# Kernel optimization log

Measured on AMD Instinct MI355X. Metric: run time of the kernel, lower is better.

The kernel has to match this reference:

```python
import jax, jax.numpy as jnp
import numpy as np

SEQ, BS, DIM = 2048, 2, 256
G, NQ = 2, 8           # n_keys groups, n_queries total
SUB = NQ // G          # queries per group
EPS = 1e-5


def _ln(x, gamma, beta):
    m = jnp.mean(x, axis=-1, keepdims=True)
    v = jnp.mean(jnp.square(x - m), axis=-1, keepdims=True)
    return (x - m) * jax.lax.rsqrt(v + EPS) * gamma + beta


def setup_inputs() -> dict:
    key = jax.random.key(0)
    ks = jax.random.split(key, 16)
    s = 0.02
    return {
        "x":   jax.random.normal(ks[0], (SEQ, BS, DIM), jnp.float32),
        # block layernorms
        "g0": jnp.ones((DIM,), jnp.float32), "b0": jnp.zeros((DIM,), jnp.float32),
        "g1": jnp.ones((DIM,), jnp.float32), "b1": jnp.zeros((DIM,), jnp.float32),
        # attention q/k layernorm (norm_kvs=True)
        "gn": jnp.ones((DIM,), jnp.float32), "bn": jnp.zeros((DIM,), jnp.float32),
        # attention projections (torch Linear: weight [out,in])
        "wk": jax.random.normal(ks[1], (DIM * G, DIM), jnp.float32) * s,
        "bk": jnp.zeros((DIM * G,), jnp.float32),
        "wv": jax.random.normal(ks[2], (DIM * G, DIM), jnp.float32) * s,
        "bv": jnp.zeros((DIM * G,), jnp.float32),
        "wq": jax.random.normal(ks[3], (DIM * NQ, DIM), jnp.float32) * s,
        "bq": jnp.zeros((DIM * NQ,), jnp.float32),
        "wo": jax.random.normal(ks[4], (DIM, DIM * NQ), jnp.float32) * s,
        "bo": jnp.zeros((DIM,), jnp.float32),
        # FFN: BayesLora(dim,2dim) -> relu -> BayesLora(2dim,dim), eval == plain linear
        "w1": jax.random.normal(ks[5], (2 * DIM, DIM), jnp.float32) * s,
        "bf1": jnp.zeros((2 * DIM,), jnp.float32),
        "w2": jax.random.normal(ks[6], (DIM, 2 * DIM), jnp.float32) * s,
        "bf2": jnp.zeros((DIM,), jnp.float32),
    }


def reference(x, g0, b0, g1, b1, gn, bn, wk, bk, wv, bv, wq, bq, wo, bo, w1, bf1, w2, bf2):
    seq, bs, dim = x.shape
    # --- attention (pre-norm) ---
    h = _ln(x, g0, b0)                                        # s b d
    K = (h @ wk.T + bk).reshape(seq, bs, G, dim)              # s b g i
    V = (h @ wv.T + bv).reshape(seq, bs, G, dim)              # s b g i
    Q = (h @ wq.T + bq).reshape(seq, bs, G, SUB, dim)         # s b g u i
    K = _ln(K, gn, bn)
    Q = _ln(Q, gn, bn)
    scores = jnp.einsum('sbgui,tbgi->bgust', Q, K) / jnp.sqrt(jnp.float32(dim))
    neg = jnp.finfo(scores.dtype).min
    causal = jnp.tril(jnp.ones((seq, seq), bool))             # s1 >= s2 allowed
    scores = jnp.where(causal, scores, neg)
    probs = jax.nn.softmax(scores, axis=-1)                   # b g u s t
    out = jnp.einsum('bgust,tbgi->sbgui', probs, V)
    out = out.reshape(seq, bs, G * SUB * dim)                 # s b (g u i)
    x = x + (out @ wo.T + bo)
    # --- FFN (pre-norm) ---
    h2 = _ln(x, g1, b1)
    f = jax.nn.relu(h2 @ w1.T + bf1) @ w2.T + bf2
    return x + f
```

## Files before the change

### kernel.cpp

```cpp
#include <hip/hip_runtime.h>
#include <hip/hip_bf16.h>

#define SEQ  2048
#define BSZ  2
#define DIM  256
#define NG   2
#define NQH  8
#define SUBQ 4
#define ROWS (SEQ*BSZ)
#define NQKV 3072
#define QROW 6144

typedef unsigned int uint32;
typedef unsigned short ushort;
typedef __attribute__((ext_vector_type(8))) short short8;
typedef __attribute__((ext_vector_type(4))) float f32x4;

__device__ __forceinline__ float bflo(uint32 u){
  union { uint32 i; float f; } c; c.i = u << 16; return c.f;
}
__device__ __forceinline__ float bfhi(uint32 u){
  union { uint32 i; float f; } c; c.i = u & 0xffff0000u; return c.f;
}
__device__ __forceinline__ uint32 pack2(float a, float b){
  __hip_bfloat16 ha = __float2bfloat16(a);
  __hip_bfloat16 hb = __float2bfloat16(b);
  unsigned short ua, ub;
  __builtin_memcpy(&ua, &ha, 2);
  __builtin_memcpy(&ub, &hb, 2);
  return (uint32)ua | ((uint32)ub << 16);
}
__device__ __forceinline__ ushort bf16bits(float v){
  __hip_bfloat16 h = __float2bfloat16(v);
  ushort u; __builtin_memcpy(&u, &h, 2); return u;
}

__device__ __forceinline__ void dma16(const void* g, void* l) {
  __builtin_amdgcn_global_load_lds(
      (const __attribute__((address_space(1))) uint32*)g,
      (__attribute__((address_space(3))) uint32*)l, 16, 0, 0);
}

__device__ __forceinline__ size_t op2_addr(size_t o2) {
  return (o2 >> 11) * QROW + (o2 & 1023) + ((o2 >> 10) & 1) * 3072;
}

__global__ __launch_bounds__(256) void misc0(
    const float* __restrict__ wk, const float* __restrict__ wv,
    const float* __restrict__ wq, const float* __restrict__ wo,
    const float* __restrict__ w1, const float* __restrict__ w2,
    const float* __restrict__ bk, const float* __restrict__ bv,
    const float* __restrict__ bq,
    __hip_bfloat16* __restrict__ out, float* __restrict__ bc,
    const float* __restrict__ x, const float* __restrict__ g0,
    const float* __restrict__ b0, __hip_bfloat16* __restrict__ Hf)
{
  if (blockIdx.x < 771) {
    int u = blockIdx.x * 256 + threadIdx.x;
    if (u < 196608) {
      int lane = u & 63, col = lane & 15, quad = lane >> 4;
      const float* srcrow;
      if (u < 98304) {
        int n16 = u >> 9, kc = (u >> 6) & 7;
        int n = n16 * 16 + col;
        const float* m = (n < 512) ? (wk + (size_t)n * 256)
                       : (n < 1024) ? (wv + (size_t)(n - 512) * 256)
                                    : (wq + (size_t)(n - 1024) * 256);
        srcrow = m + kc * 32 + quad * 8;
      } else if (u < 163840) {
        int local = u - 98304;
        int n16 = local >> 12, kc = (local >> 6) & 63;
        srcrow = wo + (size_t)(n16 * 16 + col) * 2048 + kc * 32 + quad * 8;
      } else if (u < 180224) {
        int local = u - 163840;
        int n16 = local >> 9, kc = (local >> 6) & 7;
        srcrow = w1 + (size_t)(n16 * 16 + col) * 256 + kc * 32 + quad * 8;
      } else {
        int local = u - 180224;
        int n16 = local >> 10, kc = (local >> 6) & 15;
        srcrow = w2 + (size_t)(n16 * 16 + col) * 512 + kc * 32 + quad * 8;
      }
      float4 a = *(const float4*)srcrow;
      float4 b = *(const float4*)(srcrow + 4);
      uint4 st;
      st.x = pack2(a.x, a.y); st.y = pack2(a.z, a.w);
      st.z = pack2(b.x, b.y); st.w = pack2(b.z, b.w);
      *(uint4*)((ushort*)out + (size_t)u * 8) = st;
    } else {
      int bu = u - 196608;
      const float* src; int loc;
      if      (bu < 128) { src = bk; loc = bu; }
      else if (bu < 256) { src = bv; loc = bu - 128; }
      else               { src = bq; loc = bu - 256; }
      *(float4*)(bc + 4 * (size_t)bu) = *(const float4*)(src + 4 * (size_t)loc);
    }
  } else {
    int wave = threadIdx.x >> 6, lane = threadIdx.x & 63;
    int row = (blockIdx.x - 771) * 4 + wave;
    size_t base = (size_t)row * DIM + lane * 4;
    float4 v = *(const float4*)(x + base);
    float s  = v.x + v.y + v.z + v.w;
    float s2 = v.x*v.x + v.y*v.y + v.z*v.z + v.w*v.w;
    #pragma unroll
    for (int o = 1; o < 64; o <<= 1) {
      s  += __shfl_xor(s, o);
      s2 += __shfl_xor(s2, o);
    }
    float m = s * (1.0f / DIM);
    float rb = rsqrtf(s2 * (1.0f / DIM) - m * m + 1e-5f);
    float4 gm = *(const float4*)(g0 + lane * 4);
    float4 bt = *(const float4*)(b0 + lane * 4);
    uint2 st;
    st.x = pack2((v.x - m) * rb * gm.x + bt.x, (v.y - m) * rb * gm.y + bt.y);
    st.y = pack2((v.z - m) * rb * gm.z + bt.z, (v.w - m) * rb * gm.w + bt.w);
    int kc = lane >> 3, quad = (lane >> 1) & 3, jj = 4 * (lane & 1);
    int cid = (row >> 4) * 8 + kc;
    *(uint2*)((ushort*)Hf + (size_t)cid * 512 + (quad * 16 + (row & 15)) * 8 + jj) = st;
  }
}

__global__ __launch_bounds__(256) void ln_swz(
    __hip_bfloat16* __restrict__ QKV,
    const float* __restrict__ gamma, const float* __restrict__ beta,
    __hip_bfloat16* __restrict__ Kf, __hip_bfloat16* __restrict__ Vf)
{
  int j = blockIdx.x;
  if (j < 10240) {
    int wave = threadIdx.x >> 6, lane = threadIdx.x & 63;
    int idx = j * 4 + wave;
    size_t base;
    if (idx < 8192) base = (size_t)(idx >> 1) * NQKV + (idx & 1) * DIM;
    else {
      int qi = idx - 8192;
      base = (size_t)(qi >> 3) * NQKV + 2 * NG * DIM + (qi & 7) * DIM;
    }
    __hip_bfloat16* p = QKV + base + lane * 4;
    uint2 u = *(const uint2*)p;
    float v0 = bflo(u.x), v1 = bfhi(u.x), v2 = bflo(u.y), v3 = bfhi(u.y);
    float s  = v0 + v1 + v2 + v3;
    float s2 = v0*v0 + v1*v1 + v2*v2 + v3*v3;
    #pragma unroll
    for (int o = 1; o < 64; o <<= 1) {
      s  += __shfl_xor(s, o);
      s2 += __shfl_xor(s2, o);
    }
    float m = s * (1.0f / DIM);
    float rb = rsqrtf(s2 * (1.0f / DIM) - m * m + 1e-5f);
    float4 gm = *(const float4*)(gamma + lane * 4);
    float4 bt = *(const float4*)(beta + lane * 4);
    uint2 st;
    st.x = pack2((v0 - m) * rb * gm.x + bt.x, (v1 - m) * rb * gm.y + bt.y);
    st.y = pack2((v2 - m) * rb * gm.z + bt.z, (v3 - m) * rb * gm.w + bt.w);
    if (idx < 8192) {
      int r = idx >> 1, gg = idx & 1;
      int t = r >> 1, b = r & 1;
      int bg = b * NG + gg;
      int kt = t >> 5, tr = t & 31, tc = tr >> 4, col = tr & 15;
      int ks = lane >> 3, quad = (lane >> 1) & 3, jj = 4 * (lane & 1);
      int cid = (bg * 64 + kt) * 16 + tc * 8 + ks;
      *(uint2*)((ushort*)Kf + (size_t)cid * 512 + (quad * 16 + col) * 8 + jj) = st;
    } else {
      *(uint2*)p = st;
    }
  } else {
    __shared__ ushort T[64][72];
    int vb = j - 10240;
    int t0 = (vb & 31) * 64, d0 = ((vb >> 5) & 3) * 64, bg = vb >> 7;
    int b = bg >> 1, g = bg & 1;
    int tid = threadIdx.x;
    int tr = tid >> 2, c4 = (tid & 3) * 16;
    const ushort* src = (const ushort*)QKV + ((size_t)(t0 + tr) * BSZ + b) * NQKV
                      + NG * DIM + g * DIM + d0 + c4;
    uint4 a0 = *(const uint4*)src;
    uint4 a1 = *(const uint4*)(src + 8);
    *(uint4*)&T[tr][c4]     = a0;
    *(uint4*)&T[tr][c4 + 8] = a1;
    __syncthreads();
    #pragma unroll
    for (int k2 = 0; k2 < 2; ++k2) {
      int u = tid * 2 + k2;
      int tt = u >> 8, di = (u >> 6) & 3, qd = (u >> 4) & 3, cl = u & 15;
      ushort tmp[8];
      #pragma unroll
      for (int e = 0; e < 8; ++e) tmp[e] = T[tt * 32 + qd * 8 + e][di * 16 + cl];
      int kt = (t0 >> 5) + tt;
      int dc = (d0 >> 4) + di;
      *(uint4*)((ushort*)Vf + (((size_t)(bg * 64 + kt) * 16 + dc) << 9) + (qd * 16 + cl) * 8)
          = *(uint4*)tmp;
    }
  }
}

template<int GN, int RELU, int OUTMODE, int AFRAG>
__global__ __launch_bounds__(256) void gemm_mfma(
    const __hip_bfloat16* __restrict__ A,
    const __hip_bfloat16* __restrict__ W,
    const float* __restrict__ bias,
    const float* __restrict__ resid,
    void* __restrict__ outp,
    int M, int N, int K)
{
  constexpr int WCH = GN / 16;
  constexpr int MC  = (GN == 128) ? 4 : 2;
  __shared__ __align__(16) ushort AS[2][4096];
  __shared__ __align__(16) ushort WS[2][WCH * 512];

  const int tid = threadIdx.x;
  const int wave = tid >> 6, lane = tid & 63;
  const int col = lane & 15, quad = lane >> 4;
  const int wm = (GN == 128) ? (wave >> 1) : wave;
  const int wn = (GN == 128) ? (wave & 1) : 0;
  const int bn0 = blockIdx.x * GN;
  const int bm0 = blockIdx.y * 128;
  const bool SPLIT = (OUTMODE == 2 || OUTMODE == 4);
  const int Keff  = SPLIT ? (K / gridDim.z) : K;
  const int kbase = SPLIT ? blockIdx.z * Keff : 0;
  const int kiters = Keff >> 5;

  f32x4 acc[MC][4];
  #pragma unroll
  for (int mc = 0; mc < MC; ++mc)
    #pragma unroll
    for (int nc = 0; nc < 4; ++nc)
      acc[mc][nc] = (f32x4){0.f, 0.f, 0.f, 0.f};

  auto stage = [&](int it, int bufi) {
    int k0 = kbase + it * 32;
    #pragma unroll
    for (int c = 0; c < 2; ++c) {
      int ch = wave * 2 + c;
      if (AFRAG)
        dma16((const ushort*)A + ((((size_t)(bm0 >> 4) + ch) * (K >> 5) + (k0 >> 5)) << 9) + lane * 8,
              &AS[bufi][ch * 512]);
      else
        dma16((const ushort*)A + (size_t)(bm0 + ch * 16 + col) * K + k0 + quad * 8,
              &AS[bufi][ch * 512]);
    }
    #pragma unroll
    for (int c = 0; c < WCH / 4; ++c) {
      int ch = wave * (WCH / 4) + c;
      dma16((const ushort*)W + (((size_t)((bn0 >> 4) + ch) * (K >> 5) + (k0 >> 5)) << 9) + lane * 8,
            &WS[bufi][ch * 512]);
    }
  };

  stage(0, 0);
  for (int it = 0; it < kiters; ++it) {
    int cur = it & 1;
    __syncthreads();
    if (it + 1 < kiters) stage(it + 1, 1 - cur);
    short8 af[MC], bf_[4];
    #pragma unroll
    for (int mc = 0; mc < MC; ++mc)
      af[mc] = *(const short8*)&AS[cur][(wm * MC + mc) * 512 + lane * 8];
    #pragma unroll
    for (int nc = 0; nc < 4; ++nc)
      bf_[nc] = *(const short8*)&WS[cur][(wn * 4 + nc) * 512 + lane * 8];
    #pragma unroll
    for (int mc = 0; mc < MC; ++mc)
      #pragma unroll
      for (int nc = 0; nc < 4; ++nc)
        acc[mc][nc] = __builtin_amdgcn_mfma_f32_16x16x32_bf16(af[mc], bf_[nc], acc[mc][nc], 0, 0, 0);
  }

  #pragma unroll
  for (int nc = 0; nc < 4; ++nc) {
    int n = bn0 + wn * 64 + nc * 16 + col;
    float bv = 0.f;
    if (OUTMODE == 0 || OUTMODE == 1 || OUTMODE == 3) bv = bias[n];
    #pragma unroll
    for (int mc = 0; mc < MC; ++mc) {
      #pragma unroll
      for (int reg = 0; reg < 4; ++reg) {
        int m = bm0 + wm * (MC * 16) + mc * 16 + quad * 4 + reg;
        float v = acc[mc][nc][reg] + bv;
        if ((OUTMODE == 0 || OUTMODE == 1 || OUTMODE == 3) && resid)
          v += resid[(size_t)m * N + n];
        if (RELU) v = fmaxf(v, 0.f);
        if (OUTMODE == 0)
          ((__hip_bfloat16*)outp)[(size_t)m * N + n] = __float2bfloat16(v);
        else if (OUTMODE == 1)
          ((float*)outp)[(size_t)m * N + n] = v;
        else if (OUTMODE == 2)
          ((float*)outp)[(size_t)blockIdx.z * M * N + (size_t)m * N + n] = v;
        else if (OUTMODE == 3) {
          int cid = (m >> 4) * (N >> 5) + (n >> 5);
          int kl = n & 31;
          ((ushort*)outp)[(size_t)cid * 512 + ((kl >> 3) * 16 + (m & 15)) * 8 + (kl & 7)] = bf16bits(v);
        } else {
          ((ushort*)outp)[(size_t)blockIdx.z * M * N + (size_t)m * N + n] = bf16bits(v);
        }
      }
    }
  }
}

__global__ __launch_bounds__(256) void combine2(
    const ushort* __restrict__ P, const float* __restrict__ bias,
    const float* __restrict__ resid, float* __restrict__ out, int MN)
{
  int i4 = (blockIdx.x * 256 + threadIdx.x) * 4;
  uint2 a = *(const uint2*)(P + i4);
  uint2 b = *(const uint2*)(P + MN + i4);
  float4 r = *(const float4*)(resid + i4);
  float4 bb = *(const float4*)(bias + (i4 & (DIM - 1)));
  float4 o;
  o.x = bflo(a.x) + bflo(b.x) + r.x + bb.x;
  o.y = bfhi(a.x) + bfhi(b.x) + r.y + bb.y;
  o.z = bflo(a.y) + bflo(b.y) + r.z + bb.z;
  o.w = bfhi(a.y) + bfhi(b.y) + r.w + bb.w;
  *(float4*)(out + i4) = o;
}

__global__ __launch_bounds__(256) void combine_ln4(
    const ushort* __restrict__ P, const float* __restrict__ bias,
    const float* __restrict__ resid, float* __restrict__ X2,
    const float* __restrict__ gamma, const float* __restrict__ beta,
    __hip_bfloat16* __restrict__ H2f)
{
  const int MN = ROWS * DIM;
  int wave = threadIdx.x >> 6, lane = threadIdx.x & 63;
  int row = blockIdx.x * 4 + wave;
  size_t i = (size_t)row * DIM + lane * 4;
  uint2 a = *(const uint2*)(P + i);
  uint2 b = *(const uint2*)(P + MN + i);
  uint2 c = *(const uint2*)(P + 2 * (size_t)MN + i);
  uint2 d = *(const uint2*)(P + 3 * (size_t)MN + i);
  float4 r = *(const float4*)(resid + i);
  float4 bb = *(const float4*)(bias + lane * 4);
  float4 v;
  v.x = bflo(a.x) + bflo(b.x) + bflo(c.x) + bflo(d.x) + r.x + bb.x;
  v.y = bfhi(a.x) + bfhi(b.x) + bfhi(c.x) + bfhi(d.x) + r.y + bb.y;
  v.z = bflo(a.y) + bflo(b.y) + bflo(c.y) + bflo(d.y) + r.z + bb.z;
  v.w = bfhi(a.y) + bfhi(b.y) + bfhi(c.y) + bfhi(d.y) + r.w + bb.w;
  *(float4*)(X2 + i) = v;
  float s  = v.x + v.y + v.z + v.w;
  float s2 = v.x*v.x + v.y*v.y + v.z*v.z + v.w*v.w;
  #pragma unroll
  for (int o = 1; o < 64; o <<= 1) {
    s  += __shfl_xor(s, o);
    s2 += __shfl_xor(s2, o);
  }
  float m = s * (1.0f / DIM);
  float rb = rsqrtf(s2 * (1.0f / DIM) - m * m + 1e-5f);
  float4 gm = *(const float4*)(gamma + lane * 4);
  float4 bt = *(const float4*)(beta + lane * 4);
  uint2 st;
  st.x = pack2((v.x - m) * rb * gm.x + bt.x, (v.y - m) * rb * gm.y + bt.y);
  st.y = pack2((v.z - m) * rb * gm.z + bt.z, (v.w - m) * rb * gm.w + bt.w);
  int kc = lane >> 3, quad = (lane >> 1) & 3, jj = 4 * (lane & 1);
  int cid = (row >> 4) * 8 + kc;
  *(uint2*)((ushort*)H2f + (size_t)cid * 512 + (quad * 16 + (row & 15)) * 8 + jj) = st;
}

__constant__ int C_NIT[32] = {22,22,22,21,21,20,20,20,20,20,20,19,19,18,18,18,18,17,17,16,16,16,16,16,16,14,14,12,12,12, 8, 4};
__constant__ int C_QB [32] = {10,10,15,15,15, 4, 9, 9,14,14,14,13,13,13, 8, 8,12,12,12, 3, 7, 7,11,11,11, 6, 6, 2, 5, 5, 1, 0};
__constant__ int C_Z  [32] = { 0, 1, 0, 1, 2, 0, 0, 1, 0, 1, 2, 0, 1, 2, 0, 1, 0, 1, 2, 0, 0, 1, 0, 1, 2, 0, 1, 0, 0, 1, 0, 0};
__constant__ int C_K0 [32] = { 0,22, 0,22,43, 0, 0,20, 0,20,40, 0,19,38, 0,18, 0,18,35, 0, 0,16, 0,16,32, 0,14, 0, 0,12, 0, 0};
__constant__ int C_SP [32] = { 1, 1, 1, 1, 1, 0, 1, 1, 1, 1, 1, 1, 1, 1, 1, 1, 1, 1, 1, 0, 1, 1, 1, 1, 1, 1, 1, 0, 1, 1, 0, 0};

__global__ __launch_bounds__(256, 2) void attn_mfma(
    const __hip_bfloat16* QKV,
    const __hip_bfloat16* __restrict__ Kf,
    const __hip_bfloat16* __restrict__ Vf,
    __hip_bfloat16* __restrict__ Obf,
    __hip_bfloat16* __restrict__ Op1f,
    ushort* Op2q,
    float* __restrict__ Lp)
{
  __shared__ __align__(16) ushort KS[2][8192];
  __shared__ __align__(16) ushort VS[2][8192];
  __shared__ __align__(16) ushort Pw[4][1280];

  const int tid  = threadIdx.x;
  const int wave = tid >> 6, lane = tid & 63;
  const int col  = lane & 15, quad = lane >> 4;

  const int bid = blockIdx.x;
  const int x8 = bid & 7, j = bid >> 3;
  const int a = j >> 1, odd = j & 1;
  int rank;
  if (a < 16) rank = odd ? (31 - a) : a;
  else        rank = odd ? (a - 16) : (31 - (a - 16));
  const int head = odd * 8 + x8;
  const int qb  = C_QB[rank];
  const int z   = C_Z[rank];
  const int nit = C_NIT[rank];
  const int k0  = C_K0[rank];
  const int split = C_SP[rank];

  const int b = head >> 3, hq = head & 7, g = hq >> 2;
  const int bg = b * NG + g;
  const int qw0 = qb * 128 + wave * 32;

  short8 qf[2][8];
  #pragma unroll
  for (int mc = 0; mc < 2; ++mc) {
    int s = qw0 + mc * 16 + col;
    const ushort* qp = (const ushort*)QKV + (size_t)s * QROW + b * NQKV
                     + 2 * NG * DIM + hq * DIM + quad * 8;
    #pragma unroll
    for (int ks = 0; ks < 8; ++ks)
      qf[mc][ks] = *(const short8*)(qp + ks * 32);
  }

  short8 onesf;
  #pragma unroll
  for (int i = 0; i < 8; ++i) onesf[i] = (short)0x3F80;

  f32x4 o[2][16];
  #pragma unroll
  for (int mc = 0; mc < 2; ++mc)
    #pragma unroll
    for (int dc = 0; dc < 16; ++dc)
      o[mc][dc] = (f32x4){0.f, 0.f, 0.f, 0.f};
  float l_s[2][4] = {{0.f}};

  auto stage = [&](int i, int bufi) {
    int kt = k0 + i;
    const ushort* kb = (const ushort*)Kf + (((size_t)bg * 64 + kt) << 13);
    const ushort* vb = (const ushort*)Vf + (((size_t)bg * 64 + kt) << 13);
    #pragma unroll
    for (int cc = 0; cc < 4; ++cc) {
      int nk = wave * 4 + cc;
      dma16(kb + (nk << 9) + lane * 8, &KS[bufi][nk * 512]);
      dma16(vb + (nk << 9) + lane * 8, &VS[bufi][nk * 512]);
    }
  };

  stage(0, 0);
  for (int i = 0; i < nit; ++i) {
    int cur = i & 1;
    __syncthreads();
    if (i + 1 < nit) stage(i + 1, 1 - cur);
    int kt = k0 + i;
    if (kt * 32 > qw0 + 31) continue;

    f32x4 sf[2][2];
    #pragma unroll
    for (int mc = 0; mc < 2; ++mc)
      #pragma unroll
      for (int tc = 0; tc < 2; ++tc)
        sf[mc][tc] = (f32x4){0.f, 0.f, 0.f, 0.f};
    #pragma unroll
    for (int ks = 0; ks < 8; ++ks) {
      short8 kb0 = *(const short8*)&KS[cur][ks * 512 + lane * 8];
      short8 kb1 = *(const short8*)&KS[cur][(8 + ks) * 512 + lane * 8];
      sf[0][0] = __builtin_amdgcn_mfma_f32_16x16x32_bf16(qf[0][ks], kb0, sf[0][0], 0, 0, 0);
      sf[0][1] = __builtin_amdgcn_mfma_f32_16x16x32_bf16(qf[0][ks], kb1, sf[0][1], 0, 0, 0);
      sf[1][0] = __builtin_amdgcn_mfma_f32_16x16x32_bf16(qf[1][ks], kb0, sf[1][0], 0, 0, 0);
      sf[1][1] = __builtin_amdgcn_mfma_f32_16x16x32_bf16(qf[1][ks], kb1, sf[1][1], 0, 0, 0);
    }

    const bool dm = (kt * 32 + 31) > qw0;
    #pragma unroll
    for (int mc = 0; mc < 2; ++mc)
      #pragma unroll
      for (int tc = 0; tc < 2; ++tc)
        #pragma unroll
        for (int reg = 0; reg < 4; ++reg) {
          float p = __expf(sf[mc][tc][reg] * 0.0625f);
          if (dm) {
            int tg = kt * 32 + tc * 16 + col;
            int sg = qw0 + mc * 16 + quad * 4 + reg;
            if (tg > sg) p = 0.f;
          }
          Pw[wave][(mc * 16 + quad * 4 + reg) * 40 + tc * 16 + col] = bf16bits(p);
        }

    short8 pa0 = *(const short8*)&Pw[wave][col * 40 + quad * 8];
    short8 pa1 = *(const short8*)&Pw[wave][(16 + col) * 40 + quad * 8];

    f32x4 zz = (f32x4){0.f, 0.f, 0.f, 0.f};
    f32x4 ps0 = __builtin_amdgcn_mfma_f32_16x16x32_bf16(pa0, onesf, zz, 0, 0, 0);
    f32x4 ps1 = __builtin_amdgcn_mfma_f32_16x16x32_bf16(pa1, onesf, zz, 0, 0, 0);
    #pragma unroll
    for (int r = 0; r < 4; ++r) { l_s[0][r] += ps0[r]; l_s[1][r] += ps1[r]; }

    #pragma unroll
    for (int dc = 0; dc < 16; ++dc) {
      short8 vb = *(const short8*)&VS[cur][dc * 512 + lane * 8];
      o[0][dc] = __builtin_amdgcn_mfma_f32_16x16x32_bf16(pa0, vb, o[0][dc], 0, 0, 0);
      o[1][dc] = __builtin_amdgcn_mfma_f32_16x16x32_bf16(pa1, vb, o[1][dc], 0, 0, 0);
    }
  }

  const int colh = col >> 3, coll = col & 7;
  #pragma unroll
  for (int mc = 0; mc < 2; ++mc)
    #pragma unroll
    for (int reg = 0; reg < 4; ++reg) {
      int s = qw0 + mc * 16 + quad * 4 + reg;
      int m = s * BSZ + b;
      int m16 = m >> 4, ml = m & 15;
      if (!split) {
        float inv = 1.0f / l_s[mc][reg];
        #pragma unroll
        for (int dc = 0; dc < 16; ++dc) {
          int cid = m16 * 64 + hq * 8 + (dc >> 1);
          int qt = (dc & 1) * 2 + colh;
          Obf[(size_t)cid * 512 + (qt * 16 + ml) * 8 + coll] =
              __float2bfloat16(o[mc][dc][reg] * inv);
        }
      } else {
        #pragma unroll
        for (int dc = 0; dc < 16; ++dc) {
          int qt = (dc & 1) * 2 + colh;
          int el = (qt * 16 + ml) * 8 + coll;
          float v = o[mc][dc][reg];
          if (z == 0) {
            Obf[((size_t)(m16 * 64 + hq * 8 + (dc >> 1))) * 512 + el] = __float2bfloat16(v);
          } else if (z == 1) {
            Op1f[((size_t)((m16 - 80) * 64 + hq * 8 + (dc >> 1))) * 512 + el] = __float2bfloat16(v);
          } else {
            size_t o2 = ((size_t)((m16 - 176) * 64 + hq * 8 + (dc >> 1))) * 512 + el;
            Op2q[op2_addr(o2)] = bf16bits(v);
          }
        }
        if (col == 0) Lp[((size_t)z * 2048 + s) * 16 + head] = l_s[mc][reg];
      }
    }
}

__global__ __launch_bounds__(256) void attn_norm(
    __hip_bfloat16* __restrict__ Obf, const __hip_bfloat16* __restrict__ Op1f,
    const ushort* __restrict__ Op2q, const float* __restrict__ Lp)
{
  int i8 = blockIdx.x * 256 + threadIdx.x;
  int cidr = i8 >> 6;
  int lane = i8 & 63;
  int m16r = cidr >> 6, kc = cidr & 63;
  int m16 = m16r + 80;
  int m = m16 * 16 + (lane & 15);
  int k = kc * 32 + (lane >> 4) * 8;
  int s = m >> 1, b = m & 1, hq = k >> 8;
  int head = b * 8 + hq;
  float l = Lp[(size_t)s * 16 + head] + Lp[(size_t)(2048 + s) * 16 + head];
  ushort* a = (ushort*)Obf + (((size_t)m16 * 64 + kc) << 9) + lane * 8;
  const ushort* c = (const ushort*)Op1f + (((size_t)m16r * 64 + kc) << 9) + lane * 8;
  uint4 ua = *(const uint4*)a;
  uint4 uc = *(const uint4*)c;
  float v0 = bflo(ua.x) + bflo(uc.x), v1 = bfhi(ua.x) + bfhi(uc.x);
  float v2 = bflo(ua.y) + bflo(uc.y), v3 = bfhi(ua.y) + bfhi(uc.y);
  float v4 = bflo(ua.z) + bflo(uc.z), v5 = bfhi(ua.z) + bfhi(uc.z);
  float v6 = bflo(ua.w) + bflo(uc.w), v7 = bfhi(ua.w) + bfhi(uc.w);
  if (s >= 1408) {
    l += Lp[(size_t)(4096 + s) * 16 + head];
    size_t o2 = (((size_t)(m16 - 176) * 64 + kc) << 9) + lane * 8;
    uint4 ue = *(const uint4*)(Op2q + op2_addr(o2));
    v0 += bflo(ue.x); v1 += bfhi(ue.x);
    v2 += bflo(ue.y); v3 += bfhi(ue.y);
    v4 += bflo(ue.z); v5 += bfhi(ue.z);
    v6 += bflo(ue.w); v7 += bfhi(ue.w);
  }
  float inv = 1.0f / l;
  uint4 st;
  st.x = pack2(v0 * inv, v1 * inv);
  st.y = pack2(v2 * inv, v3 * inv);
  st.z = pack2(v4 * inv, v5 * inv);
  st.w = pack2(v6 * inv, v7 * inv);
  *(uint4*)a = st;
}

extern "C" void kernel_launch(void* const* d_in, const int* in_sizes, int n_in,
                              void* d_out, int out_size, void* d_ws, size_t ws_size,
                              hipStream_t stream)
{
  const float* x   = (const float*)d_in[0];
  const float* g0  = (const float*)d_in[1];
  const float* b0  = (const float*)d_in[2];
  const float* g1  = (const float*)d_in[3];
  const float* b1  = (const float*)d_in[4];
  const float* gn  = (const float*)d_in[5];
  const float* bn  = (const float*)d_in[6];
  const float* wk  = (const float*)d_in[7];
  const float* bk  = (const float*)d_in[8];
  const float* wv  = (const float*)d_in[9];
  const float* bv  = (const float*)d_in[10];
  const float* wq  = (const float*)d_in[11];
  const float* bq  = (const float*)d_in[12];
  const float* wo  = (const float*)d_in[13];
  const float* bo  = (const float*)d_in[14];
  const float* w1  = (const float*)d_in[15];
  const float* bf1 = (const float*)d_in[16];
  const float* w2  = (const float*)d_in[17];
  const float* bf2 = (const float*)d_in[18];

  char* ws = (char*)d_ws;
  const size_t MB = 1024 * 1024;
  __hip_bfloat16* QKV = (__hip_bfloat16*)(ws);
  __hip_bfloat16* Pwo = (__hip_bfloat16*)(ws);
  __hip_bfloat16* Pw2 = (__hip_bfloat16*)(ws + 8  * MB);
  float*          X2  = (float*)         (ws + 16 * MB);
  __hip_bfloat16* H2f = (__hip_bfloat16*)(ws + 20 * MB);
  __hip_bfloat16* F1f = (__hip_bfloat16*)(ws + 22 * MB);
  __hip_bfloat16* Hf  = (__hip_bfloat16*)(ws + 24 * MB);
  __hip_bfloat16* Kf  = (__hip_bfloat16*)(ws + 24 * MB);
  __hip_bfloat16* Vf  = (__hip_bfloat16*)(ws + 28 * MB);
  __hip_bfloat16* Obf = (__hip_bfloat16*)(ws + 32 * MB);
  __hip_bfloat16* Op1f= (__hip_bfloat16*)(ws + 48 * MB);
  float*          BC  = (float*)         (ws + 59 * MB);
  float*          Lp  = (float*)         (ws + 59 * MB + 64 * 1024);
  __hip_bfloat16* WB  = (__hip_bfloat16*)(ws + 61 * MB);

  __hip_bfloat16* woB = WB + 786432;
  __hip_bfloat16* w1B = WB + 1310720;
  __hip_bfloat16* w2B = WB + 1441792;

  misc0<<<1795, 256, 0, stream>>>(wk, wv, wq, wo, w1, w2, bk, bv, bq, WB, BC, x, g0, b0, Hf);
  gemm_mfma<128,0,0,1><<<dim3(NQKV/128, ROWS/128), 256, 0, stream>>>(Hf, WB, BC, nullptr, QKV, ROWS, NQKV, DIM);
  ln_swz<<<12288, 256, 0, stream>>>(QKV, gn, bn, Kf, Vf);
  attn_mfma<<<512, 256, 0, stream>>>(QKV, Kf, Vf, Obf, Op1f, (ushort*)QKV, Lp);
  attn_norm<<<2816, 256, 0, stream>>>(Obf, Op1f, (const ushort*)QKV, Lp);
  gemm_mfma<64,0,4,1><<<dim3(DIM/64, ROWS/128, 4), 256, 0, stream>>>(Obf, woB, nullptr, nullptr, Pwo, ROWS, DIM, NQH*DIM);
  combine_ln4<<<ROWS / 4, 256, 0, stream>>>((const ushort*)Pwo, bo, x, X2, g1, b1, H2f);
  gemm_mfma<64,1,3,1><<<dim3((2*DIM)/64, ROWS/128), 256, 0, stream>>>(H2f, w1B, bf1, nullptr, F1f, ROWS, 2*DIM, DIM);
  gemm_mfma<64,0,4,1><<<dim3(DIM/64, ROWS/128, 2), 256, 0, stream>>>(F1f, w2B, nullptr, nullptr, Pw2, ROWS, DIM, 2*DIM);
  combine2<<<ROWS*DIM/1024, 256, 0, stream>>>((const ushort*)Pw2, bf2, X2, (float*)d_out, ROWS*DIM);
}
```

Measured before the change: 241.9 us.

## Fuse Q layernorm into attention kernel and raise MFMA wave priority

Removes the Q-layernorm pass from ln_swz (grid shrinks from 12288 to 4096 blocks) and instead normalizes Q fragments in registers at the start of attn_mfma, using cross-lane shuffles for mean and variance. This drops a read-modify-write of the 16 MB Q region of the QKV buffer. It also wraps the QK and PV MFMA loops in s_setprio(1)/s_setprio(0) so waves issuing matrix ops get scheduler priority. The cost is that each attention block recomputes Q norms, and the extra gamma/beta loads add some register pressure.

Result: slower. 253.8 us (+4.9%).

```diff
diff --git a/kernel.cpp b/kernel.cpp
--- a/kernel.cpp
+++ b/kernel.cpp
@@ -21,6 +21,9 @@
 }
 __device__ __forceinline__ float bfhi(uint32 u){
   union { uint32 i; float f; } c; c.i = u & 0xffff0000u; return c.f;
+}
+__device__ __forceinline__ float bfu(ushort u){
+  union { uint32 i; float f; } c; c.i = (uint32)u << 16; return c.f;
 }
 __device__ __forceinline__ uint32 pack2(float a, float b){
   __hip_bfloat16 ha = __float2bfloat16(a);
@@ -125,15 +128,10 @@
     __hip_bfloat16* __restrict__ Kf, __hip_bfloat16* __restrict__ Vf)
 {
   int j = blockIdx.x;
-  if (j < 10240) {
+  if (j < 2048) {
     int wave = threadIdx.x >> 6, lane = threadIdx.x & 63;
     int idx = j * 4 + wave;
-    size_t base;
-    if (idx < 8192) base = (size_t)(idx >> 1) * NQKV + (idx & 1) * DIM;
-    else {
-      int qi = idx - 8192;
-      base = (size_t)(qi >> 3) * NQKV + 2 * NG * DIM + (qi & 7) * DIM;
-    }
+    size_t base = (size_t)(idx >> 1) * NQKV + (idx & 1) * DIM;
     __hip_bfloat16* p = QKV + base + lane * 4;
     uint2 u = *(const uint2*)p;
     float v0 = bflo(u.x), v1 = bfhi(u.x), v2 = bflo(u.y), v3 = bfhi(u.y);
@@ -151,20 +149,16 @@
     uint2 st;
     st.x = pack2((v0 - m) * rb * gm.x + bt.x, (v1 - m) * rb * gm.y + bt.y);
     st.y = pack2((v2 - m) * rb * gm.z + bt.z, (v3 - m) * rb * gm.w + bt.w);
-    if (idx < 8192) {
-      int r = idx >> 1, gg = idx & 1;
-      int t = r >> 1, b = r & 1;
-      int bg = b * NG + gg;
-      int kt = t >> 5, tr = t & 31, tc = tr >> 4, col = tr & 15;
-      int ks = lane >> 3, quad = (lane >> 1) & 3, jj = 4 * (lane & 1);
-      int cid = (bg * 64 + kt) * 16 + tc * 8 + ks;
-      *(uint2*)((ushort*)Kf + (size_t)cid * 512 + (quad * 16 + col) * 8 + jj) = st;
-    } else {
-      *(uint2*)p = st;
-    }
+    int r = idx >> 1, gg = idx & 1;
+    int t = r >> 1, b = r & 1;
+    int bg = b * NG + gg;
+    int kt = t >> 5, tr = t & 31, tc = tr >> 4, col = tr & 15;
+    int ks = lane >> 3, quad = (lane >> 1) & 3, jj = 4 * (lane & 1);
+    int cid = (bg * 64 + kt) * 16 + tc * 8 + ks;
+    *(uint2*)((ushort*)Kf + (size_t)cid * 512 + (quad * 16 + col) * 8 + jj) = st;
   } else {
     __shared__ ushort T[64][72];
-    int vb = j - 10240;
+    int vb = j - 2048;
     int t0 = (vb & 31) * 64, d0 = ((vb >> 5) & 3) * 64, bg = vb >> 7;
     int b = bg >> 1, g = bg & 1;
     int tid = threadIdx.x;
@@ -363,6 +357,7 @@
     const __hip_bfloat16* QKV,
     const __hip_bfloat16* __restrict__ Kf,
     const __hip_bfloat16* __restrict__ Vf,
+    const float* __restrict__ gn, const float* __restrict__ bn,
     __hip_bfloat16* __restrict__ Obf,
     __hip_bfloat16* __restrict__ Op1f,
     ushort* Op2q,
@@ -402,6 +397,32 @@
     #pragma unroll
     for (int ks = 0; ks < 8; ++ks)
       qf[mc][ks] = *(const short8*)(qp + ks * 32);
+    float sm = 0.f, s2 = 0.f;
+    #pragma unroll
+    for (int ks = 0; ks < 8; ++ks)
+      #pragma unroll
+      for (int jj = 0; jj < 8; ++jj) {
+        float f = bfu((ushort)qf[mc][ks][jj]);
+        sm += f; s2 += f * f;
+      }
+    sm += __shfl_xor(sm, 16); s2 += __shfl_xor(s2, 16);
+    sm += __shfl_xor(sm, 32); s2 += __shfl_xor(s2, 32);
+    float mm = sm * (1.0f / DIM);
+    float rb = rsqrtf(s2 * (1.0f / DIM) - mm * mm + 1e-5f);
+    #pragma unroll
+    for (int ks = 0; ks < 8; ++ks) {
+      float4 ga = *(const float4*)(gn + ks * 32 + quad * 8);
+      float4 gb = *(const float4*)(gn + ks * 32 + quad * 8 + 4);
+      float4 ba = *(const float4*)(bn + ks * 32 + quad * 8);
+      float4 bb = *(const float4*)(bn + ks * 32 + quad * 8 + 4);
+      float gg[8] = {ga.x, ga.y, ga.z, ga.w, gb.x, gb.y, gb.z, gb.w};
+      float bt[8] = {ba.x, ba.y, ba.z, ba.w, bb.x, bb.y, bb.z, bb.w};
+      short8 q = qf[mc][ks];
+      #pragma unroll
+      for (int jj = 0; jj < 8; ++jj)
+        q[jj] = (short)bf16bits((bfu((ushort)q[jj]) - mm) * rb * gg[jj] + bt[jj]);
+      qf[mc][ks] = q;
+    }
   }
 
   short8 onesf;
@@ -442,6 +463,7 @@
       #pragma unroll
       for (int tc = 0; tc < 2; ++tc)
         sf[mc][tc] = (f32x4){0.f, 0.f, 0.f, 0.f};
+    __builtin_amdgcn_s_setprio(1);
     #pragma unroll
     for (int ks = 0; ks < 8; ++ks) {
       short8 kb0 = *(const short8*)&KS[cur][ks * 512 + lane * 8];
@@ -451,6 +473,7 @@
       sf[1][0] = __builtin_amdgcn_mfma_f32_16x16x32_bf16(qf[1][ks], kb0, sf[1][0], 0, 0, 0);
       sf[1][1] = __builtin_amdgcn_mfma_f32_16x16x32_bf16(qf[1][ks], kb1, sf[1][1], 0, 0, 0);
     }
+    __builtin_amdgcn_s_setprio(0);
 
     const bool dm = (kt * 32 + 31) > qw0;
     #pragma unroll
@@ -471,6 +494,7 @@
     short8 pa0 = *(const short8*)&Pw[wave][col * 40 + quad * 8];
     short8 pa1 = *(const short8*)&Pw[wave][(16 + col) * 40 + quad * 8];
 
+    __builtin_amdgcn_s_setprio(1);
     f32x4 zz = (f32x4){0.f, 0.f, 0.f, 0.f};
     f32x4 ps0 = __builtin_amdgcn_mfma_f32_16x16x32_bf16(pa0, onesf, zz, 0, 0, 0);
     f32x4 ps1 = __builtin_amdgcn_mfma_f32_16x16x32_bf16(pa1, onesf, zz, 0, 0, 0);
@@ -483,6 +507,7 @@
       o[0][dc] = __builtin_amdgcn_mfma_f32_16x16x32_bf16(pa0, vb, o[0][dc], 0, 0, 0);
       o[1][dc] = __builtin_amdgcn_mfma_f32_16x16x32_bf16(pa1, vb, o[1][dc], 0, 0, 0);
     }
+    __builtin_amdgcn_s_setprio(0);
   }
 
   const int colh = col >> 3, coll = col & 7;
@@ -609,8 +634,8 @@
 
   misc0<<<1795, 256, 0, stream>>>(wk, wv, wq, wo, w1, w2, bk, bv, bq, WB, BC, x, g0, b0, Hf);
   gemm_mfma<128,0,0,1><<<dim3(NQKV/128, ROWS/128), 256, 0, stream>>>(Hf, WB, BC, nullptr, QKV, ROWS, NQKV, DIM);
-  ln_swz<<<12288, 256, 0, stream>>>(QKV, gn, bn, Kf, Vf);
-  attn_mfma<<<512, 256, 0, stream>>>(QKV, Kf, Vf, Obf, Op1f, (ushort*)QKV, Lp);
+  ln_swz<<<4096, 256, 0, stream>>>(QKV, gn, bn, Kf, Vf);
+  attn_mfma<<<512, 256, 0, stream>>>(QKV, Kf, Vf, gn, bn, Obf, Op1f, (ushort*)QKV, Lp);
   attn_norm<<<2816, 256, 0, stream>>>(Obf, Op1f, (const ushort*)QKV, Lp);
   gemm_mfma<64,0,4,1><<<dim3(DIM/64, ROWS/128, 4), 256, 0, stream>>>(Obf, woB, nullptr, nullptr, Pwo, ROWS, DIM, NQH*DIM);
   combine_ln4<<<ROWS / 4, 256, 0, stream>>>((const ushort*)Pwo, bo, x, X2, g1, b1, H2f);
```

## Compute transposed scores and shuffle P into MFMA A-operand instead of LDS round-trip

Applied to the files above, without the earlier changes.

The QK^T MFMA now uses swapped operands so each lane holds scores laid out by key, packs probabilities to bf16 pairs in registers, and rearranges them into the A-operand layout for the PV MFMA with cross-lane shuffles. This removes the per-wave LDS write/read staging buffer for P and frees shared memory. It also wraps MFMA phases in s_setprio to favor matrix issue across waves. The cost is extra shuffle (ds_bpermute) instructions and selects per iteration, and the mask indices had to be remapped to match the transposed layout.

Measured after the change: 239.7 us. No clear change (-0.9%).

```diff
diff --git a/kernel.cpp b/kernel.cpp
--- a/kernel.cpp
+++ b/kernel.cpp
@@ -370,7 +370,6 @@
 {
   __shared__ __align__(16) ushort KS[2][8192];
   __shared__ __align__(16) ushort VS[2][8192];
-  __shared__ __align__(16) ushort Pw[4][1280];
 
   const int tid  = threadIdx.x;
   const int wave = tid >> 6, lane = tid & 63;
@@ -428,6 +427,9 @@
     }
   };
 
+  const int sig0 = col + 16 * ((quad & 1) * 2);
+  const int sig1 = sig0 + 16;
+
   stage(0, 0);
   for (int i = 0; i < nit; ++i) {
     int cur = i & 1;
@@ -442,47 +444,66 @@
       #pragma unroll
       for (int tc = 0; tc < 2; ++tc)
         sf[mc][tc] = (f32x4){0.f, 0.f, 0.f, 0.f};
+    __builtin_amdgcn_s_setprio(1);
     #pragma unroll
     for (int ks = 0; ks < 8; ++ks) {
       short8 kb0 = *(const short8*)&KS[cur][ks * 512 + lane * 8];
       short8 kb1 = *(const short8*)&KS[cur][(8 + ks) * 512 + lane * 8];
-      sf[0][0] = __builtin_amdgcn_mfma_f32_16x16x32_bf16(qf[0][ks], kb0, sf[0][0], 0, 0, 0);
-      sf[0][1] = __builtin_amdgcn_mfma_f32_16x16x32_bf16(qf[0][ks], kb1, sf[0][1], 0, 0, 0);
-      sf[1][0] = __builtin_amdgcn_mfma_f32_16x16x32_bf16(qf[1][ks], kb0, sf[1][0], 0, 0, 0);
-      sf[1][1] = __builtin_amdgcn_mfma_f32_16x16x32_bf16(qf[1][ks], kb1, sf[1][1], 0, 0, 0);
-    }
+      sf[0][0] = __builtin_amdgcn_mfma_f32_16x16x32_bf16(kb0, qf[0][ks], sf[0][0], 0, 0, 0);
+      sf[0][1] = __builtin_amdgcn_mfma_f32_16x16x32_bf16(kb1, qf[0][ks], sf[0][1], 0, 0, 0);
+      sf[1][0] = __builtin_amdgcn_mfma_f32_16x16x32_bf16(kb0, qf[1][ks], sf[1][0], 0, 0, 0);
+      sf[1][1] = __builtin_amdgcn_mfma_f32_16x16x32_bf16(kb1, qf[1][ks], sf[1][1], 0, 0, 0);
+    }
+    __builtin_amdgcn_s_setprio(0);
 
     const bool dm = (kt * 32 + 31) > qw0;
+    uint32 PK[2][2][2];
     #pragma unroll
     for (int mc = 0; mc < 2; ++mc)
       #pragma unroll
-      for (int tc = 0; tc < 2; ++tc)
+      for (int tc = 0; tc < 2; ++tc) {
+        float p[4];
         #pragma unroll
         for (int reg = 0; reg < 4; ++reg) {
-          float p = __expf(sf[mc][tc][reg] * 0.0625f);
+          p[reg] = __expf(sf[mc][tc][reg] * 0.0625f);
           if (dm) {
-            int tg = kt * 32 + tc * 16 + col;
-            int sg = qw0 + mc * 16 + quad * 4 + reg;
-            if (tg > sg) p = 0.f;
+            int tg = kt * 32 + tc * 16 + quad * 4 + reg;
+            int sg = qw0 + mc * 16 + col;
+            if (tg > sg) p[reg] = 0.f;
           }
-          Pw[wave][(mc * 16 + quad * 4 + reg) * 40 + tc * 16 + col] = bf16bits(p);
         }
-
-    short8 pa0 = *(const short8*)&Pw[wave][col * 40 + quad * 8];
-    short8 pa1 = *(const short8*)&Pw[wave][(16 + col) * 40 + quad * 8];
-
+        PK[mc][tc][0] = pack2(p[0], p[1]);
+        PK[mc][tc][1] = pack2(p[2], p[3]);
+      }
+
+    short8 pa[2];
+    #pragma unroll
+    for (int mc = 0; mc < 2; ++mc) {
+      union { uint32 u[4]; short8 s8; } cvt;
+      #pragma unroll
+      for (int dw = 0; dw < 4; ++dw) {
+        int src = (dw < 2) ? sig0 : sig1;
+        uint32 a0 = (uint32)__shfl((int)PK[mc][0][dw & 1], src, 64);
+        uint32 a1 = (uint32)__shfl((int)PK[mc][1][dw & 1], src, 64);
+        cvt.u[dw] = (quad < 2) ? a0 : a1;
+      }
+      pa[mc] = cvt.s8;
+    }
+
+    __builtin_amdgcn_s_setprio(1);
     f32x4 zz = (f32x4){0.f, 0.f, 0.f, 0.f};
-    f32x4 ps0 = __builtin_amdgcn_mfma_f32_16x16x32_bf16(pa0, onesf, zz, 0, 0, 0);
-    f32x4 ps1 = __builtin_amdgcn_mfma_f32_16x16x32_bf16(pa1, onesf, zz, 0, 0, 0);
+    f32x4 ps0 = __builtin_amdgcn_mfma_f32_16x16x32_bf16(pa[0], onesf, zz, 0, 0, 0);
+    f32x4 ps1 = __builtin_amdgcn_mfma_f32_16x16x32_bf16(pa[1], onesf, zz, 0, 0, 0);
     #pragma unroll
     for (int r = 0; r < 4; ++r) { l_s[0][r] += ps0[r]; l_s[1][r] += ps1[r]; }
 
     #pragma unroll
     for (int dc = 0; dc < 16; ++dc) {
       short8 vb = *(const short8*)&VS[cur][dc * 512 + lane * 8];
-      o[0][dc] = __builtin_amdgcn_mfma_f32_16x16x32_bf16(pa0, vb, o[0][dc], 0, 0, 0);
-      o[1][dc] = __builtin_amdgcn_mfma_f32_16x16x32_bf16(pa1, vb, o[1][dc], 0, 0, 0);
-    }
+      o[0][dc] = __builtin_amdgcn_mfma_f32_16x16x32_bf16(pa[0], vb, o[0][dc], 0, 0, 0);
+      o[1][dc] = __builtin_amdgcn_mfma_f32_16x16x32_bf16(pa[1], vb, o[1][dc], 0, 0, 0);
+    }
+    __builtin_amdgcn_s_setprio(0);
   }
 
   const int colh = col >> 3, coll = col & 7;
```
